# Optimization experiments

Measured on AMD Instinct MI355X. Metric: run time of the kernel, lower is better.

Reference implementation:

```python
import jax, jax.numpy as jnp
import numpy as np
from functools import partial

D, H, O = 4, 64, 2  # input_dim, hidden_dim, output_dim


def lstm_layer(x, Wih, Whh, bih, bhh):
    """Single PyTorch-convention LSTM layer. x: [B,T,Din] -> [B,T,H].
    Gate order i,f,g,o; weights Wih:[4H,Din], Whh:[4H,H]."""
    B = x.shape[0]
    Hd = Whh.shape[1]
    # precompute input contribution for all timesteps (one big GEMM)
    xg = jnp.einsum('btd,gd->btg', x, Wih) + bih + bhh  # [B,T,4H]

    def step(carry, xg_t):
        h, c = carry
        g = xg_t + h @ Whh.T  # [B,4H]
        i, f, gg, o = jnp.split(g, 4, axis=-1)
        i = jax.nn.sigmoid(i)
        f = jax.nn.sigmoid(f)
        gg = jnp.tanh(gg)
        o = jax.nn.sigmoid(o)
        c = f * c + i * gg
        h = o * jnp.tanh(c)
        return (h, c), h

    h0 = jnp.zeros((B, Hd), x.dtype)
    c0 = jnp.zeros((B, Hd), x.dtype)
    (_, _), hs = jax.lax.scan(step, (h0, c0), jnp.swapaxes(xg, 0, 1))  # hs: [T,B,H]
    return jnp.swapaxes(hs, 0, 1)


def setup_inputs() -> dict:
    key = jax.random.key(0)
    ks = jax.random.split(key, 13)
    s_ih0 = 1.0 / np.sqrt(H)
    inp = {
        'x': jax.random.normal(ks[0], (16384, 100, D), jnp.float32),
        'W_ih0': jax.random.uniform(ks[1], (4 * H, D), jnp.float32, -s_ih0, s_ih0),
        'W_hh0': jax.random.uniform(ks[2], (4 * H, H), jnp.float32, -s_ih0, s_ih0),
        'b_ih0': jax.random.uniform(ks[3], (4 * H,), jnp.float32, -s_ih0, s_ih0),
        'b_hh0': jax.random.uniform(ks[4], (4 * H,), jnp.float32, -s_ih0, s_ih0),
        'W_ih1': jax.random.uniform(ks[5], (4 * H, H), jnp.float32, -s_ih0, s_ih0),
        'W_hh1': jax.random.uniform(ks[6], (4 * H, H), jnp.float32, -s_ih0, s_ih0),
        'b_ih1': jax.random.uniform(ks[7], (4 * H,), jnp.float32, -s_ih0, s_ih0),
        'b_hh1': jax.random.uniform(ks[8], (4 * H,), jnp.float32, -s_ih0, s_ih0),
        'gamma': jnp.ones((H,), jnp.float32),
        'beta': jnp.zeros((H,), jnp.float32),
        'W_fc': jax.random.uniform(ks[9], (O, H), jnp.float32, -s_ih0, s_ih0),
        'b_fc': jax.random.uniform(ks[10], (O,), jnp.float32, -s_ih0, s_ih0),
    }
    return inp


def reference(x, W_ih0, W_hh0, b_ih0, b_hh0, W_ih1, W_hh1, b_ih1, b_hh1,
              gamma, beta, W_fc, b_fc):
    h1 = lstm_layer(x, W_ih0, W_hh0, b_ih0, b_hh0)   # [B,T,H]
    h2 = lstm_layer(h1, W_ih1, W_hh1, b_ih1, b_hh1)  # [B,T,H] (dropout off: eval)
    last = h2[:, -1, :]                              # [B,H]
    mu = jnp.mean(last, axis=-1, keepdims=True)
    var = jnp.mean((last - mu) ** 2, axis=-1, keepdims=True)
    normed = (last - mu) * jax.lax.rsqrt(var + 1e-5) * gamma + beta
    return normed @ W_fc.T + b_fc                    # [B,2]
```

## Files before the change

kernel.cpp:

```cpp
#include <hip/hip_runtime.h>

#define TSTEPS 100
#define BC     16
#define NBLK   (16384/BC)

typedef __attribute__((ext_vector_type(8))) short bf16x8;
typedef __attribute__((ext_vector_type(4))) short s16x4;
typedef __attribute__((ext_vector_type(4))) float f32x4;
typedef __attribute__((ext_vector_type(2))) float f32x2;

#define WS_WHH0_U 0
#define WS_WIH1_U 16384
#define WS_WHH1_U 32768
#define WS_WIH0_U 49152
#define WS_B0_F   28672
#define WS_B1_F   28928
#define WS_XF_U   65536
#define WS_NEED   (131072 + (size_t)NBLK * TSTEPS * 64 * 2)

#define MFMA(A,B,C) __builtin_amdgcn_mfma_f32_16x16x32_bf16(A,B,C,0,0,0)
#define LOG2E 1.4426950408889634f

__device__ __forceinline__ unsigned short f2bf_rne(float f) {
    unsigned int u = __float_as_uint(f);
    u += 0x7fffu + ((u >> 16) & 1u);
    return (unsigned short)(u >> 16);
}
__device__ __forceinline__ unsigned short f2bf(float f) {
    return (unsigned short)((__float_as_uint(f) + 0x8000u) >> 16);
}
__device__ __forceinline__ f32x2 exp2v(f32x2 y) {
    return (f32x2){__builtin_amdgcn_exp2f(y.x), __builtin_amdgcn_exp2f(y.y)};
}
__device__ __forceinline__ f32x2 rcpv(f32x2 y) {
    return (f32x2){__builtin_amdgcn_rcpf(y.x), __builtin_amdgcn_rcpf(y.y)};
}
__device__ __forceinline__ f32x2 sigv(f32x2 y) {
    return rcpv((f32x2){1.f, 1.f} + exp2v(y));
}
__device__ __forceinline__ f32x2 tanhv(f32x2 y) {
    const f32x2 e = exp2v(y);
    return (f32x2){1.f, 1.f} - (f32x2){2.f, 2.f} * rcpv(e + (f32x2){1.f, 1.f});
}
__device__ __forceinline__ void bar_lds() {
    asm volatile("s_waitcnt lgkmcnt(0)\n\ts_barrier" ::: "memory");
}

__global__ void reorder_w(const float* __restrict__ Wih0, const float* __restrict__ Whh0,
                          const float* __restrict__ bih0, const float* __restrict__ bhh0,
                          const float* __restrict__ Wih1, const float* __restrict__ Whh1,
                          const float* __restrict__ bih1, const float* __restrict__ bhh1,
                          unsigned short* __restrict__ wsu, float* __restrict__ wsf)
{
    const int idx = blockIdx.x * 256 + threadIdx.x;
    if (idx < 16384) {
        const int j = idx & 7, lane = (idx >> 3) & 63, kc = (idx >> 9) & 1,
                  G = (idx >> 10) & 3, ug = (idx >> 12) & 3;
        const int row = G * 64 + ug * 16 + (lane & 15);
        const int k   = kc * 32 + (lane >> 4) * 8 + j;
        wsu[WS_WHH0_U + idx] = f2bf_rne(Whh0[row * 64 + k]);
        wsu[WS_WIH1_U + idx] = f2bf_rne(Wih1[row * 64 + k]);
        wsu[WS_WHH1_U + idx] = f2bf_rne(Whh1[row * 64 + k]);
    }
    if (idx < 8192) {
        const int j = idx & 7, lane = (idx >> 3) & 63, G = (idx >> 9) & 3, ug = (idx >> 11) & 3;
        const int row = G * 64 + ug * 16 + (lane & 15);
        const float v = ((lane >> 4) == 0 && j < 4) ? Wih0[row * 4 + j] : 0.0f;
        wsu[WS_WIH0_U + idx] = f2bf_rne(v);
    }
    if (idx < 256) {
        wsf[WS_B0_F + idx] = bih0[idx] + bhh0[idx];
        wsf[WS_B1_F + idx] = bih1[idx] + bhh1[idx];
    }
}

__global__ void prep_xfrag(const float* __restrict__ x, unsigned short* __restrict__ xf) {
    const int idx = blockIdx.x * 256 + threadIdx.x;
    const int t    = idx % TSTEPS;
    const int m    = (idx / TSTEPS) & 15;
    const int tile = idx / (TSTEPS * 16);
    const float4 v = *(const float4*)(x + ((size_t)(tile * 16 + m) * TSTEPS + t) * 4);
    const s16x4 o = {(short)f2bf_rne(v.x), (short)f2bf_rne(v.y),
                     (short)f2bf_rne(v.z), (short)f2bf_rne(v.w)};
    *(s16x4*)(xf + ((size_t)(tile * TSTEPS + t) * 16 + m) * 4) = o;
}

#define L0STEP(K, P)                                                             \
  {                                                                              \
    bf16x8 ax;                                                                   \
    if (XPRE) { U8 u; u.p.lo = xv; u.p.hi = xv; ax = u.v8; }                     \
    else {                                                                       \
      ax = zfrag;                                                                \
      if (lg == 0) {                                                             \
        ax[0] = (short)f2bf_rne(xf4.x); ax[1] = (short)f2bf_rne(xf4.y);          \
        ax[2] = (short)f2bf_rne(xf4.z); ax[3] = (short)f2bf_rne(xf4.w);          \
      }                                                                          \
    }                                                                            \
    f32x4 acc0[4];                                                               \
    _Pragma("unroll") for (int G = 0; G < 4; ++G) {                              \
      acc0[G] = MFMA(A0[0], Bhh0[G][0], zero4);                                  \
      acc0[G] = MFMA(A0[1], Bhh0[G][1], acc0[G]);                                \
      acc0[G] = MFMA(ax,    Bih0[G],    acc0[G]);                                \
    }                                                                            \
    if ((K) + 1 < TSTEPS) {                                                      \
      if (XPRE) xv  = *(const s16x4*)(xfp + ((K) + 1) * 64);                     \
      else      xf4 = *(const float4*)(xb + ((K) + 1) * 4);                      \
    }                                                                            \
    _Pragma("unroll") for (int p = 0; p < 2; ++p) {                              \
      const f32x2 ig = sigv ((f32x2){acc0[0][2*p], acc0[0][2*p+1]} * nL2 + lb[0]); \
      const f32x2 fg = sigv ((f32x2){acc0[1][2*p], acc0[1][2*p+1]} * nL2 + lb[1]); \
      const f32x2 gg = tanhv((f32x2){acc0[2][2*p], acc0[2][2*p+1]} * L22 + lb[2]); \
      const f32x2 og = sigv ((f32x2){acc0[3][2*p], acc0[3][2*p+1]} * nL2 + lb[3]); \
      const f32x2 c  = fg * c0v[p] + ig * gg;                                    \
      c0v[p] = c;                                                                \
      const f32x2 h = og * tanhv(c * L22);                                       \
      *(unsigned short*)(HBc + ((P)<<11) + wbase + (2*p)  *16) = f2bf(h.x);      \
      *(unsigned short*)(HBc + ((P)<<11) + wbase + (2*p+1)*16) = f2bf(h.y);      \
    }                                                                            \
    bar_lds();                                                                   \
    A0[0] = *(const bf16x8*)(HBc + ((P)<<11) + rbase);                           \
    A0[1] = *(const bf16x8*)(HBc + ((P)<<11) + rbase + 1024);                    \
  }

#define L1STEP(J, P)                                                             \
  {                                                                              \
    f32x4 acc1[4];                                                               \
    _Pragma("unroll") for (int G = 0; G < 4; ++G) {                              \
      acc1[G] = MFMA(A0[0], Bih1[G][0], zero4);                                  \
      acc1[G] = MFMA(A0[1], Bih1[G][1], acc1[G]);                                \
      acc1[G] = MFMA(A1[0], Bhh1[G][0], acc1[G]);                                \
      acc1[G] = MFMA(A1[1], Bhh1[G][1], acc1[G]);                                \
    }                                                                            \
    _Pragma("unroll") for (int p = 0; p < 2; ++p) {                              \
      const f32x2 ig = sigv ((f32x2){acc1[0][2*p], acc1[0][2*p+1]} * nL2 + lb[0]); \
      const f32x2 fg = sigv ((f32x2){acc1[1][2*p], acc1[1][2*p+1]} * nL2 + lb[1]); \
      const f32x2 gg = tanhv((f32x2){acc1[2][2*p], acc1[2][2*p+1]} * L22 + lb[2]); \
      const f32x2 og = sigv ((f32x2){acc1[3][2*p], acc1[3][2*p+1]} * nL2 + lb[3]); \
      const f32x2 c  = fg * c1v[p] + ig * gg;                                    \
      c1v[p] = c;                                                                \
      const f32x2 h = og * tanhv(c * L22);                                       \
      *(unsigned short*)(HBc + 4096 + ((P)<<11) + wbase + (2*p)  *16) = f2bf(h.x); \
      *(unsigned short*)(HBc + 4096 + ((P)<<11) + wbase + (2*p+1)*16) = f2bf(h.y); \
    }                                                                            \
    bar_lds();                                                                   \
    A0[0] = *(const bf16x8*)(HBc + (((P)^1)<<11) + rbase);                       \
    A0[1] = *(const bf16x8*)(HBc + (((P)^1)<<11) + rbase + 1024);                \
    A1[0] = *(const bf16x8*)(HBc + 4096 + ((P)<<11) + rbase);                    \
    A1[1] = *(const bf16x8*)(HBc + 4096 + ((P)<<11) + rbase + 1024);             \
  }

template<bool XPRE>
__global__ __launch_bounds__(512, 4) void lstm2_mfma(
    const float* __restrict__ x,
    const unsigned short* __restrict__ wsu, const float* __restrict__ wsf,
    const float* __restrict__ gam, const float* __restrict__ bet,
    const float* __restrict__ Wfc, const float* __restrict__ bfc,
    float* __restrict__ out)
{
    __shared__ __align__(16) unsigned short HB[4096];
    __shared__ float H1F[BC * 65];

    const int tid  = threadIdx.x;
    const int lane = tid & 63;
    const int wv   = __builtin_amdgcn_readfirstlane(tid >> 6);
    const int ug   = wv & 3;
    const int ln15 = lane & 15, lg = lane >> 4;
    const int bblk = blockIdx.x * BC;

    const int kcw = ug >> 1;
    const int lgc = ((ug & 1) << 1) + (ln15 >> 3);
    const unsigned wbase = (unsigned)(kcw * 1024 + lgc * 256 + lg * 64 + (ln15 & 7) * 2);
    const unsigned rbase = (unsigned)(lane * 16);
    char* const HBc = (char*)HB;

    const f32x2 nL2 = {-LOG2E, -LOG2E};
    const f32x2 L22 = {2.0f * LOG2E, 2.0f * LOG2E};
    const f32x4 zero4 = {0.f, 0.f, 0.f, 0.f};
    const bf16x8 zfrag = {0,0,0,0,0,0,0,0};

    union U8 { bf16x8 v8; struct { s16x4 lo, hi; } p; };

    if (wv < 4) {
        bf16x8 Bhh0[4][2], Bih0[4];
        #pragma unroll
        for (int G = 0; G < 4; ++G) {
            #pragma unroll
            for (int kc = 0; kc < 2; ++kc)
                Bhh0[G][kc] = *(const bf16x8*)(wsu + WS_WHH0_U + (((ug*4+G)*2+kc)*512 + lane*8));
            Bih0[G] = *(const bf16x8*)(wsu + WS_WIH0_U + (ug*4+G)*512 + lane*8);
        }
        f32x2 lb[4];
        #pragma unroll
        for (int G = 0; G < 4; ++G) {
            const float b0 = wsf[WS_B0_F + G * 64 + ug * 16 + ln15];
            const float s0 = (G == 2) ? (2.0f * LOG2E) * b0 : -LOG2E * b0;
            lb[G] = (f32x2){s0, s0};
        }
        f32x2 c0v[2] = {{0.f,0.f},{0.f,0.f}};
        bf16x8 A0[2]; A0[0] = zfrag; A0[1] = zfrag;

        const unsigned short* xfp = wsu + WS_XF_U + (size_t)blockIdx.x * (TSTEPS * 64) + ln15 * 4;
        const float* xb = x + (size_t)(bblk + ln15) * (TSTEPS * 4);
        s16x4 xv = {0,0,0,0};
        float4 xf4;
        if (XPRE) xv = *(const s16x4*)(xfp);
        else      xf4 = *(const float4*)(xb);

        int k = 0;
        #pragma unroll 1
        for (int kb = 0; kb < TSTEPS / 2; ++kb) {
            L0STEP(k, 0);
            L0STEP(k + 1, 1);
            k += 2;
        }
        bar_lds();

        if (tid < BC) {
            const int b = tid;
            float hr[64];
            float mu = 0.f;
            #pragma unroll
            for (int q = 0; q < 64; ++q) { hr[q] = H1F[b * 65 + q]; mu += hr[q]; }
            mu *= (1.f / 64.f);
            float var = 0.f;
            #pragma unroll
            for (int q = 0; q < 64; ++q) { const float d = hr[q] - mu; var = fmaf(d, d, var); }
            var *= (1.f / 64.f);
            const float rs = rsqrtf(var + 1e-5f);
            float o0 = bfc[0], o1 = bfc[1];
            #pragma unroll
            for (int q = 0; q < 64; ++q) {
                const float nk = (hr[q] - mu) * rs * gam[q] + bet[q];
                o0 = fmaf(nk, Wfc[q],      o0);
                o1 = fmaf(nk, Wfc[64 + q], o1);
            }
            out[(size_t)(bblk + b) * 2 + 0] = o0;
            out[(size_t)(bblk + b) * 2 + 1] = o1;
        }
    } else {
        bf16x8 Bih1[4][2], Bhh1[4][2];
        #pragma unroll
        for (int G = 0; G < 4; ++G) {
            #pragma unroll
            for (int kc = 0; kc < 2; ++kc) {
                const int f = ((ug * 4 + G) * 2 + kc) * 512 + lane * 8;
                Bih1[G][kc] = *(const bf16x8*)(wsu + WS_WIH1_U + f);
                Bhh1[G][kc] = *(const bf16x8*)(wsu + WS_WHH1_U + f);
            }
        }
        f32x2 lb[4];
        #pragma unroll
        for (int G = 0; G < 4; ++G) {
            const float b1 = wsf[WS_B1_F + G * 64 + ug * 16 + ln15];
            const float s1 = (G == 2) ? (2.0f * LOG2E) * b1 : -LOG2E * b1;
            lb[G] = (f32x2){s1, s1};
        }
        f32x2 c1v[2] = {{0.f,0.f},{0.f,0.f}};
        bf16x8 A0[2], A1[2];
        A1[0] = zfrag; A1[1] = zfrag;

        bar_lds();
        A0[0] = *(const bf16x8*)(HBc + rbase);
        A0[1] = *(const bf16x8*)(HBc + rbase + 1024);

        int j = 0;
        #pragma unroll 1
        for (int jb = 0; jb < (TSTEPS - 2) / 2; ++jb) {
            L1STEP(j, 0);
            L1STEP(j + 1, 1);
            j += 2;
        }
        L1STEP(98, 0);

        {
            f32x4 acc1[4];
            #pragma unroll
            for (int G = 0; G < 4; ++G) {
                acc1[G] = MFMA(A0[0], Bih1[G][0], zero4);
                acc1[G] = MFMA(A0[1], Bih1[G][1], acc1[G]);
                acc1[G] = MFMA(A1[0], Bhh1[G][0], acc1[G]);
                acc1[G] = MFMA(A1[1], Bhh1[G][1], acc1[G]);
            }
            #pragma unroll
            for (int p = 0; p < 2; ++p) {
                const f32x2 ig = sigv ((f32x2){acc1[0][2*p], acc1[0][2*p+1]} * nL2 + lb[0]);
                const f32x2 fg = sigv ((f32x2){acc1[1][2*p], acc1[1][2*p+1]} * nL2 + lb[1]);
                const f32x2 gg = tanhv((f32x2){acc1[2][2*p], acc1[2][2*p+1]} * L22 + lb[2]);
                const f32x2 og = sigv ((f32x2){acc1[3][2*p], acc1[3][2*p+1]} * nL2 + lb[3]);
                const f32x2 c  = fg * c1v[p] + ig * gg;
                c1v[p] = c;
                const f32x2 h = og * tanhv(c * L22);
                H1F[(lg * 4 + 2*p)     * 65 + ug * 16 + ln15] = h.x;
                H1F[(lg * 4 + 2*p + 1) * 65 + ug * 16 + ln15] = h.y;
            }
        }
        bar_lds();
    }
}

extern "C" void kernel_launch(void* const* d_in, const int* in_sizes, int n_in,
                              void* d_out, int out_size, void* d_ws, size_t ws_size,
                              hipStream_t stream) {
    (void)in_sizes; (void)n_in; (void)out_size;
    const float* x    = (const float*)d_in[0];
    const float* Wih0 = (const float*)d_in[1];
    const float* Whh0 = (const float*)d_in[2];
    const float* bih0 = (const float*)d_in[3];
    const float* bhh0 = (const float*)d_in[4];
    const float* Wih1 = (const float*)d_in[5];
    const float* Whh1 = (const float*)d_in[6];
    const float* bih1 = (const float*)d_in[7];
    const float* bhh1 = (const float*)d_in[8];
    const float* gam  = (const float*)d_in[9];
    const float* bet  = (const float*)d_in[10];
    const float* Wfc  = (const float*)d_in[11];
    const float* bfc  = (const float*)d_in[12];
    unsigned short* wsu = (unsigned short*)d_ws;
    float*          wsf = (float*)d_ws;
    float* out = (float*)d_out;

    hipLaunchKernelGGL(reorder_w, dim3(96), dim3(256), 0, stream,
                       Wih0, Whh0, bih0, bhh0, Wih1, Whh1, bih1, bhh1, wsu, wsf);
    if (ws_size >= WS_NEED) {
        hipLaunchKernelGGL(prep_xfrag, dim3(NBLK * 16 * TSTEPS / 256), dim3(256), 0, stream,
                           x, wsu + WS_XF_U);
        hipLaunchKernelGGL((lstm2_mfma<true>), dim3(NBLK), dim3(512), 0, stream,
                           x, wsu, wsf, gam, bet, Wfc, bfc, out);
    } else {
        hipLaunchKernelGGL((lstm2_mfma<false>), dim3(NBLK), dim3(512), 0, stream,
                           x, wsu, wsf, gam, bet, Wfc, bfc, out);
    }
}
```

Baseline: 277.5 us.

## Fold activation scales into weights, bias into MFMA accumulator, merge gate reciprocals

The log2e and -2log2e scaling factors are pre-multiplied into the bf16 weights and biases during reordering. The bias now seeds the MFMA accumulator, so no per-gate multiply-add is needed after the matrix product. The LSTM cell is rewritten algebraically so the sigmoid and tanh reciprocals collapse into two reciprocals per element instead of five. Launch bounds drop from 4 to 3 waves per SIMD, which allows more registers but lowers occupancy. Folding the scale before bf16 rounding shifts rounding error, and the products of exponentials can overflow for large pre-activations.

```diff
diff --git a/kernel.cpp b/kernel.cpp
--- a/kernel.cpp
+++ b/kernel.cpp
@@ -35,13 +35,22 @@
 __device__ __forceinline__ f32x2 rcpv(f32x2 y) {
     return (f32x2){__builtin_amdgcn_rcpf(y.x), __builtin_amdgcn_rcpf(y.y)};
 }
-__device__ __forceinline__ f32x2 sigv(f32x2 y) {
-    return rcpv((f32x2){1.f, 1.f} + exp2v(y));
-}
-__device__ __forceinline__ f32x2 tanhv(f32x2 y) {
-    const f32x2 e = exp2v(y);
-    return (f32x2){1.f, 1.f} - (f32x2){2.f, 2.f} * rcpv(e + (f32x2){1.f, 1.f});
-}
+
+__device__ __forceinline__ f32x2 lstm_cell(f32x2 yi, f32x2 yf, f32x2 yg, f32x2 yo,
+                                           f32x2& c) {
+    const f32x2 one = {1.f, 1.f};
+    const f32x2 L22 = {2.0f * LOG2E, 2.0f * LOG2E};
+    const f32x2 Ei = exp2v(yi), Ef = exp2v(yf), Eg = exp2v(yg), Eo = exp2v(yo);
+    const f32x2 t1 = Ei + one, t2 = Ef + one, t3 = Eg + one, t4 = Eg - one;
+    const f32x2 u  = t1 * t3;
+    const f32x2 R1 = rcpv(u * t2);
+    c = (c * u + t4 * t2) * R1;
+    const f32x2 Ec = exp2v(c * L22);
+    const f32x2 t5 = Ec - one, t6 = Ec + one, t7 = Eo + one;
+    const f32x2 R2 = rcpv(t7 * t6);
+    return t5 * R2;
+}
+
 __device__ __forceinline__ void bar_lds() {
     asm volatile("s_waitcnt lgkmcnt(0)\n\ts_barrier" ::: "memory");
 }
@@ -58,19 +67,23 @@
                   G = (idx >> 10) & 3, ug = (idx >> 12) & 3;
         const int row = G * 64 + ug * 16 + (lane & 15);
         const int k   = kc * 32 + (lane >> 4) * 8 + j;
-        wsu[WS_WHH0_U + idx] = f2bf_rne(Whh0[row * 64 + k]);
-        wsu[WS_WIH1_U + idx] = f2bf_rne(Wih1[row * 64 + k]);
-        wsu[WS_WHH1_U + idx] = f2bf_rne(Whh1[row * 64 + k]);
+        const float sc = (G == 2) ? (2.0f * LOG2E) : -LOG2E;
+        wsu[WS_WHH0_U + idx] = f2bf_rne(sc * Whh0[row * 64 + k]);
+        wsu[WS_WIH1_U + idx] = f2bf_rne(sc * Wih1[row * 64 + k]);
+        wsu[WS_WHH1_U + idx] = f2bf_rne(sc * Whh1[row * 64 + k]);
     }
     if (idx < 8192) {
         const int j = idx & 7, lane = (idx >> 3) & 63, G = (idx >> 9) & 3, ug = (idx >> 11) & 3;
         const int row = G * 64 + ug * 16 + (lane & 15);
-        const float v = ((lane >> 4) == 0 && j < 4) ? Wih0[row * 4 + j] : 0.0f;
+        const float sc = (G == 2) ? (2.0f * LOG2E) : -LOG2E;
+        const float v = ((lane >> 4) == 0 && j < 4) ? sc * Wih0[row * 4 + j] : 0.0f;
         wsu[WS_WIH0_U + idx] = f2bf_rne(v);
     }
     if (idx < 256) {
-        wsf[WS_B0_F + idx] = bih0[idx] + bhh0[idx];
-        wsf[WS_B1_F + idx] = bih1[idx] + bhh1[idx];
+        const int G = idx >> 6;
+        const float sc = (G == 2) ? (2.0f * LOG2E) : -LOG2E;
+        wsf[WS_B0_F + idx] = sc * (bih0[idx] + bhh0[idx]);
+        wsf[WS_B1_F + idx] = sc * (bih1[idx] + bhh1[idx]);
     }
 }
 
@@ -88,7 +101,7 @@
 #define L0STEP(K, P)                                                             \
   {                                                                              \
     bf16x8 ax;                                                                   \
-    if (XPRE) { U8 u; u.p.lo = xv; u.p.hi = xv; ax = u.v8; }                     \
+    if (XPRE) { U8 u_; u_.p.lo = xv; u_.p.hi = xv; ax = u_.v8; }                 \
     else {                                                                       \
       ax = zfrag;                                                                \
       if (lg == 0) {                                                             \
@@ -98,7 +111,7 @@
     }                                                                            \
     f32x4 acc0[4];                                                               \
     _Pragma("unroll") for (int G = 0; G < 4; ++G) {                              \
-      acc0[G] = MFMA(A0[0], Bhh0[G][0], zero4);                                  \
+      acc0[G] = MFMA(A0[0], Bhh0[G][0], bV[G]);                                  \
       acc0[G] = MFMA(A0[1], Bhh0[G][1], acc0[G]);                                \
       acc0[G] = MFMA(ax,    Bih0[G],    acc0[G]);                                \
     }                                                                            \
@@ -107,13 +120,11 @@
       else      xf4 = *(const float4*)(xb + ((K) + 1) * 4);                      \
     }                                                                            \
     _Pragma("unroll") for (int p = 0; p < 2; ++p) {                              \
-      const f32x2 ig = sigv ((f32x2){acc0[0][2*p], acc0[0][2*p+1]} * nL2 + lb[0]); \
-      const f32x2 fg = sigv ((f32x2){acc0[1][2*p], acc0[1][2*p+1]} * nL2 + lb[1]); \
-      const f32x2 gg = tanhv((f32x2){acc0[2][2*p], acc0[2][2*p+1]} * L22 + lb[2]); \
-      const f32x2 og = sigv ((f32x2){acc0[3][2*p], acc0[3][2*p+1]} * nL2 + lb[3]); \
-      const f32x2 c  = fg * c0v[p] + ig * gg;                                    \
-      c0v[p] = c;                                                                \
-      const f32x2 h = og * tanhv(c * L22);                                       \
+      const f32x2 h = lstm_cell(                                                 \
+        (f32x2){acc0[0][2*p], acc0[0][2*p+1]},                                   \
+        (f32x2){acc0[1][2*p], acc0[1][2*p+1]},                                   \
+        (f32x2){acc0[2][2*p], acc0[2][2*p+1]},                                   \
+        (f32x2){acc0[3][2*p], acc0[3][2*p+1]}, c0v[p]);                          \
       *(unsigned short*)(HBc + ((P)<<11) + wbase + (2*p)  *16) = f2bf(h.x);      \
       *(unsigned short*)(HBc + ((P)<<11) + wbase + (2*p+1)*16) = f2bf(h.y);      \
     }                                                                            \
@@ -126,19 +137,17 @@
   {                                                                              \
     f32x4 acc1[4];                                                               \
     _Pragma("unroll") for (int G = 0; G < 4; ++G) {                              \
-      acc1[G] = MFMA(A0[0], Bih1[G][0], zero4);                                  \
+      acc1[G] = MFMA(A0[0], Bih1[G][0], bV[G]);                                  \
       acc1[G] = MFMA(A0[1], Bih1[G][1], acc1[G]);                                \
       acc1[G] = MFMA(A1[0], Bhh1[G][0], acc1[G]);                                \
       acc1[G] = MFMA(A1[1], Bhh1[G][1], acc1[G]);                                \
     }                                                                            \
     _Pragma("unroll") for (int p = 0; p < 2; ++p) {                              \
-      const f32x2 ig = sigv ((f32x2){acc1[0][2*p], acc1[0][2*p+1]} * nL2 + lb[0]); \
-      const f32x2 fg = sigv ((f32x2){acc1[1][2*p], acc1[1][2*p+1]} * nL2 + lb[1]); \
-      const f32x2 gg = tanhv((f32x2){acc1[2][2*p], acc1[2][2*p+1]} * L22 + lb[2]); \
-      const f32x2 og = sigv ((f32x2){acc1[3][2*p], acc1[3][2*p+1]} * nL2 + lb[3]); \
-      const f32x2 c  = fg * c1v[p] + ig * gg;                                    \
-      c1v[p] = c;                                                                \
-      const f32x2 h = og * tanhv(c * L22);                                       \
+      const f32x2 h = lstm_cell(                                                 \
+        (f32x2){acc1[0][2*p], acc1[0][2*p+1]},                                   \
+        (f32x2){acc1[1][2*p], acc1[1][2*p+1]},                                   \
+        (f32x2){acc1[2][2*p], acc1[2][2*p+1]},                                   \
+        (f32x2){acc1[3][2*p], acc1[3][2*p+1]}, c1v[p]);                          \
       *(unsigned short*)(HBc + 4096 + ((P)<<11) + wbase + (2*p)  *16) = f2bf(h.x); \
       *(unsigned short*)(HBc + 4096 + ((P)<<11) + wbase + (2*p+1)*16) = f2bf(h.y); \
     }                                                                            \
@@ -150,7 +159,7 @@
   }
 
 template<bool XPRE>
-__global__ __launch_bounds__(512, 4) void lstm2_mfma(
+__global__ __launch_bounds__(512, 3) void lstm2_mfma(
     const float* __restrict__ x,
     const unsigned short* __restrict__ wsu, const float* __restrict__ wsf,
     const float* __restrict__ gam, const float* __restrict__ bet,
@@ -173,11 +182,7 @@
     const unsigned rbase = (unsigned)(lane * 16);
     char* const HBc = (char*)HB;
 
-    const f32x2 nL2 = {-LOG2E, -LOG2E};
-    const f32x2 L22 = {2.0f * LOG2E, 2.0f * LOG2E};
-    const f32x4 zero4 = {0.f, 0.f, 0.f, 0.f};
     const bf16x8 zfrag = {0,0,0,0,0,0,0,0};
-
     union U8 { bf16x8 v8; struct { s16x4 lo, hi; } p; };
 
     if (wv < 4) {
@@ -189,12 +194,11 @@
                 Bhh0[G][kc] = *(const bf16x8*)(wsu + WS_WHH0_U + (((ug*4+G)*2+kc)*512 + lane*8));
             Bih0[G] = *(const bf16x8*)(wsu + WS_WIH0_U + (ug*4+G)*512 + lane*8);
         }
-        f32x2 lb[4];
+        f32x4 bV[4];
         #pragma unroll
         for (int G = 0; G < 4; ++G) {
-            const float b0 = wsf[WS_B0_F + G * 64 + ug * 16 + ln15];
-            const float s0 = (G == 2) ? (2.0f * LOG2E) * b0 : -LOG2E * b0;
-            lb[G] = (f32x2){s0, s0};
+            const float b = wsf[WS_B0_F + G * 64 + ug * 16 + ln15];
+            bV[G] = (f32x4){b, b, b, b};
         }
         f32x2 c0v[2] = {{0.f,0.f},{0.f,0.f}};
         bf16x8 A0[2]; A0[0] = zfrag; A0[1] = zfrag;
@@ -248,12 +252,11 @@
                 Bhh1[G][kc] = *(const bf16x8*)(wsu + WS_WHH1_U + f);
             }
         }
-        f32x2 lb[4];
+        f32x4 bV[4];
         #pragma unroll
         for (int G = 0; G < 4; ++G) {
-            const float b1 = wsf[WS_B1_F + G * 64 + ug * 16 + ln15];
-            const float s1 = (G == 2) ? (2.0f * LOG2E) * b1 : -LOG2E * b1;
-            lb[G] = (f32x2){s1, s1};
+            const float b = wsf[WS_B1_F + G * 64 + ug * 16 + ln15];
+            bV[G] = (f32x4){b, b, b, b};
         }
         f32x2 c1v[2] = {{0.f,0.f},{0.f,0.f}};
         bf16x8 A0[2], A1[2];
@@ -276,20 +279,18 @@
             f32x4 acc1[4];
             #pragma unroll
             for (int G = 0; G < 4; ++G) {
-                acc1[G] = MFMA(A0[0], Bih1[G][0], zero4);
+                acc1[G] = MFMA(A0[0], Bih1[G][0], bV[G]);
                 acc1[G] = MFMA(A0[1], Bih1[G][1], acc1[G]);
                 acc1[G] = MFMA(A1[0], Bhh1[G][0], acc1[G]);
                 acc1[G] = MFMA(A1[1], Bhh1[G][1], acc1[G]);
             }
             #pragma unroll
             for (int p = 0; p < 2; ++p) {
-                const f32x2 ig = sigv ((f32x2){acc1[0][2*p], acc1[0][2*p+1]} * nL2 + lb[0]);
-                const f32x2 fg = sigv ((f32x2){acc1[1][2*p], acc1[1][2*p+1]} * nL2 + lb[1]);
-                const f32x2 gg = tanhv((f32x2){acc1[2][2*p], acc1[2][2*p+1]} * L22 + lb[2]);
-                const f32x2 og = sigv ((f32x2){acc1[3][2*p], acc1[3][2*p+1]} * nL2 + lb[3]);
-                const f32x2 c  = fg * c1v[p] + ig * gg;
-                c1v[p] = c;
-                const f32x2 h = og * tanhv(c * L22);
+                const f32x2 h = lstm_cell(
+                    (f32x2){acc1[0][2*p], acc1[0][2*p+1]},
+                    (f32x2){acc1[1][2*p], acc1[1][2*p+1]},
+                    (f32x2){acc1[2][2*p], acc1[2][2*p+1]},
+                    (f32x2){acc1[3][2*p], acc1[3][2*p+1]}, c1v[p]);
                 H1F[(lg * 4 + 2*p)     * 65 + ug * 16 + ln15] = h.x;
                 H1F[(lg * 4 + 2*p + 1) * 65 + ug * 16 + ln15] = h.y;
             }
```

Result: faster. 237.7 us (-14.3%).
